# Kernel tuning notes

Measured on AMD Instinct MI355X. Metric: run time of the kernel, lower is better.

The kernel has to match this reference:

```python
import jax, jax.numpy as jnp
import numpy as np
import math

N_EDGES = 3
N_HEADS = 2
ITERS = 2
NEG = -1e9


def setup_inputs() -> dict:
    key = jax.random.key(0)
    ks = jax.random.split(key, 8)
    B, N, D = 4, 2048, 256
    E, H, I = N_EDGES, N_HEADS, ITERS
    s = 1.0 / math.sqrt(D)
    return {
        "nodes_embed": jax.random.normal(ks[0], (B, N, D), jnp.float32),
        "node_adj": jax.random.randint(ks[1], (B, N, N), 0, E + 1, jnp.int32),
        "Wq": jax.random.normal(ks[2], (E, D, D), jnp.float32) * s,
        "bq": jnp.zeros((E, D), jnp.float32),
        "Wk": jax.random.normal(ks[3], (E, D, D), jnp.float32) * s,
        "bk": jnp.zeros((E, D), jnp.float32),
        "gcn_W": jax.random.normal(ks[4], (I, D, D), jnp.float32) * s,
        "gcn_b": jnp.zeros((I, D), jnp.float32),
        "agg_W": jax.random.normal(ks[5], (H * D, D), jnp.float32) * (1.0 / math.sqrt(H * D)),
        "agg_b": jnp.zeros((D,), jnp.float32),
    }


def _forward(nodes_embed, node_adj, Wq, bq, Wk, bk, gcn_W, gcn_b, agg_W, agg_b):
    B, N, D = nodes_embed.shape
    H = N_HEADS
    dk = D // H
    adj = node_adj[:, None]  # [B,1,N,N] broadcast over heads

    # Per-edge-type masked attention accumulation (scores init at 0).
    scores = jnp.zeros((B, H, N, N), nodes_embed.dtype)
    for e in range(N_EDGES):  # small fixed edge-type loop
        q = (nodes_embed @ Wq[e] + bq[e]).reshape(B, N, H, dk).transpose(0, 2, 1, 3)
        k = (nodes_embed @ Wk[e] + bk[e]).reshape(B, N, H, dk).transpose(0, 2, 1, 3)
        raw = jnp.einsum('bhnd,bhmd->bhnm', q, k) / math.sqrt(dk)
        scores = jnp.where(adj == e + 1, scores + raw, scores)

    # Positions never touched (adj==0 or no matching type) stay exactly 0 -> masked.
    scores = jnp.where(scores == 0.0, NEG, scores)
    attn = jax.nn.softmax(scores, axis=-1)  # [B,H,N,N]

    # Per-head GCN stack (parameters shared across heads, as in the torch code).
    outs = []
    for head in range(H):
        a = attn[:, head]  # [B,N,N]
        degs = jnp.sum(a, axis=-1, keepdims=True)  # [B,N,1]
        x = nodes_embed
        for i in range(ITERS):
            h1 = jnp.einsum('bnd,df->bnf', x, gcn_W[i])
            sum_nei = jnp.einsum('bnm,bmf->bnf', a, h1)
            x = x + jax.nn.relu(sum_nei / degs + gcn_b[i])
        outs.append(x)

    out = jnp.concatenate(outs, axis=-1) @ agg_W + agg_b  # [B,N,D]
    graph_attention = jnp.transpose(attn, (1, 0, 2, 3))  # [H,B,N,N]
    return out, graph_attention


def reference(nodes_embed, node_adj, Wq, bq, Wk, bk, gcn_W, gcn_b, agg_W, agg_b):
    return _forward(nodes_embed, node_adj, Wq, bq, Wk, bk, gcn_W, gcn_b, agg_W, agg_b)
```

## Files before the change

kernel.cpp:

```cpp
#include <hip/hip_runtime.h>
#include <stdint.h>
#include <stddef.h>


typedef unsigned short bf16_t;
typedef __attribute__((ext_vector_type(4))) float floatx4;
typedef __attribute__((ext_vector_type(8))) __bf16 bf16x8;
typedef __attribute__((ext_vector_type(4))) unsigned short u16x4;

__device__ __forceinline__ bf16_t f2b(float f) {
  union { float f; uint32_t u; } v; v.f = f;
  uint32_t r = v.u + 0x7FFFu + ((v.u >> 16) & 1u);
  return (bf16_t)(r >> 16);
}
__device__ __forceinline__ float h2f(uint16_t u) {
  union { uint16_t u; _Float16 h; } v; v.u = u; return (float)v.h;
}
__device__ __forceinline__ uint16_t f2h(float f) {
  union { uint16_t u; _Float16 h; } v; v.h = (_Float16)f; return v.u;
}

typedef __attribute__((address_space(1))) void gvoid_t;
typedef __attribute__((address_space(3))) void svoid_t;
__device__ __forceinline__ void gll16(const void* g, void* l) {
  __builtin_amdgcn_global_load_lds((gvoid_t*)(g), (svoid_t*)(l), 16, 0, 0);
}


template <int NR>
__device__ __forceinline__ void stage128(const bf16_t* G, int ldg, bf16_t* L) {
  const int lane = threadIdx.x & 63, wave = threadIdx.x >> 6;
  const int li = lane >> 4, cp = lane & 15;
#pragma unroll
  for (int t = 0; t < NR / 16; ++t) {
    int base_r = wave * (NR / 4) + t * 4;
    int r = base_r + li;
    int cl = cp ^ (r & 15);
    gll16(G + (size_t)r * ldg + cl * 8, L + base_r * 128);
  }
}
template <int NR>
__device__ __forceinline__ void stage64(const bf16_t* G, int ldg, bf16_t* L) {
  const int lane = threadIdx.x & 63, wave = threadIdx.x >> 6;
  const int li = lane >> 3, cp = lane & 7;
#pragma unroll
  for (int t = 0; t < NR / 32; ++t) {
    int base_r = wave * (NR / 4) + t * 8;
    int r = base_r + li;
    int cl = cp ^ (r & 7);
    gll16(G + (size_t)r * ldg + cl * 8, L + base_r * 64);
  }
}
__device__ __forceinline__ bf16x8 frag128(const bf16_t* L, int row, int j, int quad) {
  int c = ((j << 2) + quad) ^ (row & 15);
  return *(const bf16x8*)(L + (row << 7) + (c << 3));
}
__device__ __forceinline__ bf16x8 frag64(const bf16_t* L, int row, int j, int quad) {
  int c = ((j << 2) + quad) ^ (row & 7);
  return *(const bf16x8*)(L + (row << 6) + (c << 3));
}

__device__ __forceinline__ bf16x8 lds_frag(const bf16_t* base, int row, int quad) {
  return *(const bf16x8*)(base + (row << 5) + (((quad + (row >> 1)) & 3) << 3));
}
__device__ __forceinline__ void gemm_core(
    const bf16_t* __restrict__ A, int lda, int rowA0,
    const bf16_t* __restrict__ Bt, int ldb, int rowB0,
    int K, bf16_t* lA, bf16_t* lB, floatx4 acc[4][4])
{
  const int lane = threadIdx.x & 63;
  const int wave = threadIdx.x >> 6;
  const int l16  = lane & 15;
  const int quad = lane >> 4;
  const int wm = (wave >> 1) << 6;
  const int wn = (wave & 1) << 6;
  const int srow = (wave << 5) + (lane >> 2);
  const int scol = (((lane & 3) - (srow >> 1)) & 3) << 3;
  const bf16_t* gA0 = A + (size_t)(rowA0 + srow) * lda + scol;
  const bf16_t* gA1 = gA0 + (size_t)16 * lda;
  const bf16_t* gB0 = Bt + (size_t)(rowB0 + srow) * ldb + scol;
  const bf16_t* gB1 = gB0 + (size_t)16 * ldb;
  bf16_t* lA0 = lA + (wave << 5) * 32;
  bf16_t* lA1 = lA0 + 16 * 32;
  bf16_t* lB0 = lB + (wave << 5) * 32;
  bf16_t* lB1 = lB0 + 16 * 32;

  for (int k0 = 0; k0 < K; k0 += 32) {
    __syncthreads();
    gll16(gA0 + k0, lA0);
    gll16(gA1 + k0, lA1);
    gll16(gB0 + k0, lB0);
    gll16(gB1 + k0, lB1);
    __syncthreads();
    bf16x8 af[4], bv[4];
#pragma unroll
    for (int mi = 0; mi < 4; ++mi) af[mi] = lds_frag(lA, wm + mi * 16 + l16, quad);
#pragma unroll
    for (int ni = 0; ni < 4; ++ni) bv[ni] = lds_frag(lB, wn + ni * 16 + l16, quad);
#pragma unroll
    for (int mi = 0; mi < 4; ++mi)
#pragma unroll
      for (int ni = 0; ni < 4; ++ni)
        acc[mi][ni] = __builtin_amdgcn_mfma_f32_16x16x32_bf16(af[mi], bv[ni], acc[mi][ni], 0, 0, 0);
  }
}

#define TILE_IDS \
  const int lane = threadIdx.x & 63; \
  const int wave = threadIdx.x >> 6; \
  const int l16  = lane & 15; \
  const int quad = lane >> 4; \
  const int wm = (wave >> 1) << 6; \
  const int wn = (wave & 1) << 6;

#define TILE_IDS64 \
  const int lane = threadIdx.x & 63; \
  const int wave = threadIdx.x >> 6; \
  const int l16  = lane & 15; \
  const int quad = lane >> 4; \
  const int wn = wave << 5;

#define ZERO44(acc) \
  { const floatx4 z4_ = {0.f, 0.f, 0.f, 0.f}; \
    for (int mi_ = 0; mi_ < 4; ++mi_) for (int ni_ = 0; ni_ < 4; ++ni_) acc[mi_][ni_] = z4_; }
#define ZERO42(acc) \
  { const floatx4 z4_ = {0.f, 0.f, 0.f, 0.f}; \
    for (int mi_ = 0; mi_ < 4; ++mi_) for (int ni_ = 0; ni_ < 2; ++ni_) acc[mi_][ni_] = z4_; }

__global__ __launch_bounds__(256) void k_cast_x(const float* __restrict__ x,
                                                bf16_t* __restrict__ xb) {
  int i = blockIdx.x * 256 + threadIdx.x;
  float4 a = ((const float4*)x)[i * 2];
  float4 b = ((const float4*)x)[i * 2 + 1];
  bf16_t o[8] = { f2b(a.x), f2b(a.y), f2b(a.z), f2b(a.w),
                  f2b(b.x), f2b(b.y), f2b(b.z), f2b(b.w) };
  ((uint4*)xb)[i] = *(uint4*)o;
}

__global__ __launch_bounds__(256) void k_cast_w(
    const float* __restrict__ Wq, const float* __restrict__ Wk,
    const float* __restrict__ gW, const float* __restrict__ aW,
    bf16_t* __restrict__ WqkT, bf16_t* __restrict__ gWT, bf16_t* __restrict__ aWT) {
  int idx = blockIdx.x * 256 + threadIdx.x;
  if (idx < 393216) {
    int zz = idx >> 16, r = idx & 65535;
    int n = r >> 8, k = r & 255;
    const float* src = (zz < 3) ? (Wq + (size_t)zz * 65536) : (Wk + (size_t)(zz - 3) * 65536);
    WqkT[idx] = f2b(src[k * 256 + n]);
  } else if (idx < 524288) {
    int t = idx - 393216;
    int i = t >> 16, r = t & 65535;
    int f = r >> 8, k = r & 255;
    gWT[t] = f2b(gW[(size_t)i * 65536 + k * 256 + f]);
  } else if (idx < 655360) {
    int t = idx - 524288;
    int f = t >> 9, k = t & 511;
    aWT[t] = f2b(aW[k * 256 + f]);
  }
}

__global__ __launch_bounds__(256) void k_gemm_proj(
    const bf16_t* __restrict__ xb, const bf16_t* __restrict__ WqkT,
    const float* __restrict__ bq, const float* __restrict__ bk,
    bf16_t* __restrict__ qcat, bf16_t* __restrict__ kcat) {
  __shared__ bf16_t lA[4096], lB[4096];
  int z = blockIdx.z;
  int e = (z < 3) ? z : z - 3;
  const bf16_t* Wz = WqkT + (size_t)z * 65536;
  const float* bias = ((z < 3) ? bq : bk) + e * 256;
  bf16_t* dst = (z < 3) ? qcat : kcat;
  int bm0 = blockIdx.y * 128, bn0 = blockIdx.x * 128;
  floatx4 acc[4][4];
  ZERO44(acc);
  gemm_core(xb, 256, bm0, Wz, 256, bn0, 256, lA, lB, acc);
  TILE_IDS;
#pragma unroll
  for (int mi = 0; mi < 4; ++mi)
#pragma unroll
    for (int ni = 0; ni < 4; ++ni)
#pragma unroll
      for (int r = 0; r < 4; ++r) {
        int row = bm0 + wm + mi * 16 + quad * 4 + r;
        int col = bn0 + wn + ni * 16 + l16;
        int b = row >> 11, n = row & 2047;
        int h = col >> 7, kk = col & 127;
        float v = acc[mi][ni][r] + bias[col];
        dst[((size_t)((b * 2 + h) * 2048 + n)) * 384 + e * 128 + kk] = f2b(v);
      }
}

__global__ __launch_bounds__(256) void k_scores(
    const bf16_t* __restrict__ qcat, const bf16_t* __restrict__ kcat,
    const int* __restrict__ adj, uint16_t* __restrict__ sc16) {
  __shared__ bf16_t lA[64 * 128];
  __shared__ bf16_t lB[128 * 128];
  int i = blockIdx.x;
  int z = i & 7, t = i >> 3;
  int y = t & 31, x = t >> 5;
  int h = z >> 2, b = z & 3;
  const bf16_t* A  = qcat + (size_t)(b * 2 + h) * 2048 * 384;
  const bf16_t* Bt = kcat + (size_t)(b * 2 + h) * 2048 * 384;
  const int* adjb = adj + (size_t)b * 2048 * 2048;
  int bm0 = y * 64, bn0 = x * 128;
  TILE_IDS64;

  uint32_t adjv[4][2];
#pragma unroll
  for (int mi = 0; mi < 4; ++mi)
#pragma unroll
    for (int ni = 0; ni < 2; ++ni) {
      int col = bn0 + wn + ni * 16 + l16;
      uint32_t v = 0;
#pragma unroll
      for (int r = 0; r < 4; ++r) {
        int row = bm0 + mi * 16 + quad * 4 + r;
        v |= ((uint32_t)adjb[(size_t)row * 2048 + col] & 3u) << (r * 8);
      }
      adjv[mi][ni] = v;
    }

  floatx4 sel[4][2];
  ZERO42(sel);
  for (int e = 0; e < 3; ++e) {
    __syncthreads();
    stage128<64>(A + (size_t)bm0 * 384 + e * 128, 384, lA);
    stage128<128>(Bt + (size_t)bn0 * 384 + e * 128, 384, lB);
    __syncthreads();
    floatx4 acc[4][2];
    ZERO42(acc);
#pragma unroll
    for (int j = 0; j < 4; ++j) {
      bf16x8 af[4], bv[2];
#pragma unroll
      for (int mi = 0; mi < 4; ++mi) af[mi] = frag128(lA, mi * 16 + l16, j, quad);
#pragma unroll
      for (int ni = 0; ni < 2; ++ni) bv[ni] = frag128(lB, wn + ni * 16 + l16, j, quad);
#pragma unroll
      for (int mi = 0; mi < 4; ++mi)
#pragma unroll
        for (int ni = 0; ni < 2; ++ni)
          acc[mi][ni] = __builtin_amdgcn_mfma_f32_16x16x32_bf16(af[mi], bv[ni], acc[mi][ni], 0, 0, 0);
    }
#pragma unroll
    for (int mi = 0; mi < 4; ++mi)
#pragma unroll
      for (int ni = 0; ni < 2; ++ni) {
        uint32_t av = adjv[mi][ni];
#pragma unroll
        for (int r = 0; r < 4; ++r) {
          bool m = (((av >> (r * 8)) & 255u) == (uint32_t)(e + 1));
          sel[mi][ni][r] = m ? acc[mi][ni][r] : sel[mi][ni][r];
        }
      }
  }
  const float scale = 0.08838834764831845f;
#pragma unroll
  for (int mi = 0; mi < 4; ++mi)
#pragma unroll
    for (int ni = 0; ni < 2; ++ni)
#pragma unroll
      for (int r = 0; r < 4; ++r) {
        int row = bm0 + mi * 16 + quad * 4 + r;
        int col = bn0 + wn + ni * 16 + l16;
        uint32_t a = (adjv[mi][ni] >> (r * 8)) & 255u;
        float v = (a == 0u) ? -60000.0f : sel[mi][ni][r] * scale;
        sc16[((size_t)z * 2048 + row) * 2048 + col] = f2h(v);
      }
}

__global__ __launch_bounds__(256) void k_softmax(uint16_t* sb, float* attn) {
  int row = blockIdx.x * 4 + (threadIdx.x >> 6);
  int lane = threadIdx.x & 63;
  uint16_t* p = sb + (size_t)row * 2048;
  float f[32];
  float mx = -3.4e38f;
#pragma unroll
  for (int j = 0; j < 4; ++j) {
    uint4 hv = ((const uint4*)p)[j * 64 + lane];
    const uint16_t* hu = (const uint16_t*)&hv;
#pragma unroll
    for (int q = 0; q < 8; ++q) {
      float v = h2f(hu[q]);
      f[j * 8 + q] = v;
      mx = fmaxf(mx, v);
    }
  }
#pragma unroll
  for (int off = 32; off; off >>= 1) mx = fmaxf(mx, __shfl_xor(mx, off));
  float s = 0.f;
#pragma unroll
  for (int k = 0; k < 32; ++k) { f[k] = __expf(f[k] - mx); s += f[k]; }
#pragma unroll
  for (int off = 32; off; off >>= 1) s += __shfl_xor(s, off);
  float inv = 1.0f / s;
  float* ar = attn + (size_t)row * 2048;
#pragma unroll
  for (int j = 0; j < 4; ++j) {
    float o[8];
#pragma unroll
    for (int q = 0; q < 8; ++q) o[q] = f[j * 8 + q] * inv;
    ((float4*)ar)[(j * 64 + lane) * 2 + 0] = *(float4*)&o[0];
    ((float4*)ar)[(j * 64 + lane) * 2 + 1] = *(float4*)&o[4];
    uint16_t ob[8];
#pragma unroll
    for (int q = 0; q < 8; ++q) ob[q] = f2b(o[q]);
    ((uint4*)p)[j * 64 + lane] = *(uint4*)ob;
  }
}

__global__ __launch_bounds__(256) void k_gemm_bf16T(
    const bf16_t* __restrict__ A, const bf16_t* __restrict__ Wt,
    bf16_t* __restrict__ CT) {
  __shared__ bf16_t lA[4096], lB[4096];
  int bm0 = blockIdx.y * 128, bn0 = blockIdx.x * 128;
  floatx4 acc[4][4];
  ZERO44(acc);
  gemm_core(A, 256, bm0, Wt, 256, bn0, 256, lA, lB, acc);
  TILE_IDS;
#pragma unroll
  for (int mi = 0; mi < 4; ++mi)
#pragma unroll
    for (int ni = 0; ni < 4; ++ni) {
      int row0 = bm0 + wm + mi * 16 + quad * 4;
      int col  = bn0 + wn + ni * 16 + l16;
      int s = row0 >> 11, n = row0 & 2047;
      u16x4 v = { f2b(acc[mi][ni][0]), f2b(acc[mi][ni][1]),
                  f2b(acc[mi][ni][2]), f2b(acc[mi][ni][3]) };
      *(u16x4*)&CT[(size_t)s * 524288 + (size_t)col * 2048 + n] = v;
    }
}

__global__ __launch_bounds__(256) void k_spmm(
    const bf16_t* __restrict__ abf, const bf16_t* __restrict__ h1T,
    long sBb, long sBh, const float* __restrict__ bias,
    const float* __restrict__ rin, long rib, long rih,
    float* __restrict__ rout,
    bf16_t* __restrict__ obf, long obb, long obh, int ldo) {
  __shared__ bf16_t lA[64 * 64];
  __shared__ bf16_t lB[128 * 64];
  int i = blockIdx.x;
  int z = i & 7, t = i >> 3;
  int x = t & 1, y = t >> 1;
  int h = z >> 2, b = z & 3;
  const bf16_t* A  = abf + (size_t)z * 2048 * 2048;
  const bf16_t* Bt = h1T + (size_t)b * sBb + (size_t)h * sBh;
  const float* rz  = rin + (size_t)b * rib + (size_t)h * rih;
  bf16_t* oz = obf + (size_t)b * obb + (size_t)h * obh;
  int bm0 = y * 64, bn0 = x * 128;
  TILE_IDS64;
  floatx4 acc[4][2];
  ZERO42(acc);
  for (int k0 = 0; k0 < 2048; k0 += 64) {
    __syncthreads();
    stage64<64>(A + (size_t)bm0 * 2048 + k0, 2048, lA);
    stage64<128>(Bt + (size_t)bn0 * 2048 + k0, 2048, lB);
    __syncthreads();
#pragma unroll
    for (int j = 0; j < 2; ++j) {
      bf16x8 af[4], bv[2];
#pragma unroll
      for (int mi = 0; mi < 4; ++mi) af[mi] = frag64(lA, mi * 16 + l16, j, quad);
#pragma unroll
      for (int ni = 0; ni < 2; ++ni) bv[ni] = frag64(lB, wn + ni * 16 + l16, j, quad);
#pragma unroll
      for (int mi = 0; mi < 4; ++mi)
#pragma unroll
        for (int ni = 0; ni < 2; ++ni)
          acc[mi][ni] = __builtin_amdgcn_mfma_f32_16x16x32_bf16(af[mi], bv[ni], acc[mi][ni], 0, 0, 0);
    }
  }
#pragma unroll
  for (int mi = 0; mi < 4; ++mi)
#pragma unroll
    for (int ni = 0; ni < 2; ++ni)
#pragma unroll
      for (int r = 0; r < 4; ++r) {
        int row = bm0 + mi * 16 + quad * 4 + r;
        int col = bn0 + wn + ni * 16 + l16;
        float s = acc[mi][ni][r] + bias[col];
        float xn = rz[(size_t)row * 256 + col] + fmaxf(s, 0.f);
        if (rout) rout[((size_t)z * 2048 + row) * 256 + col] = xn;
        oz[(size_t)row * ldo + col] = f2b(xn);
      }
}

__global__ __launch_bounds__(256) void k_final(
    const bf16_t* __restrict__ xcat, const bf16_t* __restrict__ aWT,
    const float* __restrict__ ab, float* __restrict__ out) {
  __shared__ bf16_t lA[4096], lB[4096];
  int bm0 = blockIdx.y * 128, bn0 = blockIdx.x * 128;
  floatx4 acc[4][4];
  ZERO44(acc);
  gemm_core(xcat, 512, bm0, aWT, 512, bn0, 512, lA, lB, acc);
  TILE_IDS;
#pragma unroll
  for (int mi = 0; mi < 4; ++mi)
#pragma unroll
    for (int ni = 0; ni < 4; ++ni)
#pragma unroll
      for (int r = 0; r < 4; ++r) {
        int row = bm0 + wm + mi * 16 + quad * 4 + r;
        int col = bn0 + wn + ni * 16 + l16;
        out[(size_t)row * 256 + col] = acc[mi][ni][r] + ab[col];
      }
}

extern "C" void kernel_launch(void* const* d_in, const int* in_sizes, int n_in,
                              void* d_out, int out_size, void* d_ws, size_t ws_size,
                              hipStream_t stream) {
  const float* x   = (const float*)d_in[0];
  const int*   adj = (const int*)d_in[1];
  const float* Wq  = (const float*)d_in[2];
  const float* bq  = (const float*)d_in[3];
  const float* Wk  = (const float*)d_in[4];
  const float* bk  = (const float*)d_in[5];
  const float* gW  = (const float*)d_in[6];
  const float* gb  = (const float*)d_in[7];
  const float* aW  = (const float*)d_in[8];
  const float* ab  = (const float*)d_in[9];
  float* out = (float*)d_out;
  float* sc  = out + 2097152;

  char* w = (char*)d_ws;
  bf16_t* xb   = (bf16_t*)w; w += 4194304;
  bf16_t* WqkT = (bf16_t*)w; w += 786432;
  bf16_t* gWT  = (bf16_t*)w; w += 262144;
  bf16_t* aWT  = (bf16_t*)w; w += 262144;
  bf16_t* qcat = (bf16_t*)w; w += 12582912;
  bf16_t* kcat = (bf16_t*)w; w += 12582912;
  bf16_t* abf  = (bf16_t*)w; w += 67108864;
  bf16_t* h1T  = (bf16_t*)w; w += 4194304;
  float*  x1   = (float*)w;  w += 16777216;
  bf16_t* x1b  = (bf16_t*)w; w += 8388608;
  bf16_t* h1T1 = qcat;
  bf16_t* xcat = kcat;

  k_cast_x<<<1024, 256, 0, stream>>>(x, xb);
  k_cast_w<<<2560, 256, 0, stream>>>(Wq, Wk, gW, aW, WqkT, gWT, aWT);
  k_gemm_proj<<<dim3(2, 64, 6), 256, 0, stream>>>(xb, WqkT, bq, bk, qcat, kcat);
  k_scores<<<4096, 256, 0, stream>>>(qcat, kcat, adj, (uint16_t*)abf);
  k_softmax<<<4096, 256, 0, stream>>>((uint16_t*)abf, sc);
  k_gemm_bf16T<<<dim3(2, 64, 1), 256, 0, stream>>>(xb, gWT, h1T);
  k_spmm<<<512, 256, 0, stream>>>(abf, h1T, 524288L, 0L, gb,
                                  x, 524288L, 0L, x1,
                                  x1b, 524288L, 2097152L, 256);
  k_gemm_bf16T<<<dim3(2, 128, 1), 256, 0, stream>>>(x1b, gWT + 65536, h1T1);
  k_spmm<<<512, 256, 0, stream>>>(abf, h1T1, 524288L, 2097152L, gb + 256,
                                  x1, 524288L, 2097152L, nullptr,
                                  xcat, 1048576L, 256L, 512);
  k_final<<<dim3(2, 64, 1), 256, 0, stream>>>(xcat, aWT, ab, out);
}
```

Measured before the change: 414.7 us.

## Double-buffer LDS staging in GEMM, scores and spmm kernels; nontemporal attn stores

Converts the shared GEMM core, the scores kernel and the spmm kernel to double-buffered LDS. The next k-tile is prefetched with global_load_lds while MFMAs run on the current buffer, which drops one barrier per iteration. The scores kernel now splits each 128-wide edge slice into two 64-wide stages so all six stages share one pipelined loop. The fp32 attention output stores become nontemporal. In exchange LDS use doubles, which may reduce occupancy, and the loop correctness depends on how async LDS loads and waitcnt interact with the single barrier.

New measurement: 453.8 us. +9.4%, slower.

```diff
diff --git a/kernel.cpp b/kernel.cpp
--- a/kernel.cpp
+++ b/kernel.cpp
@@ -27,18 +27,6 @@
 }
 
 
-template <int NR>
-__device__ __forceinline__ void stage128(const bf16_t* G, int ldg, bf16_t* L) {
-  const int lane = threadIdx.x & 63, wave = threadIdx.x >> 6;
-  const int li = lane >> 4, cp = lane & 15;
-#pragma unroll
-  for (int t = 0; t < NR / 16; ++t) {
-    int base_r = wave * (NR / 4) + t * 4;
-    int r = base_r + li;
-    int cl = cp ^ (r & 15);
-    gll16(G + (size_t)r * ldg + cl * 8, L + base_r * 128);
-  }
-}
 template <int NR>
 __device__ __forceinline__ void stage64(const bf16_t* G, int ldg, bf16_t* L) {
   const int lane = threadIdx.x & 63, wave = threadIdx.x >> 6;
@@ -50,10 +38,6 @@
     int cl = cp ^ (r & 7);
     gll16(G + (size_t)r * ldg + cl * 8, L + base_r * 64);
   }
-}
-__device__ __forceinline__ bf16x8 frag128(const bf16_t* L, int row, int j, int quad) {
-  int c = ((j << 2) + quad) ^ (row & 15);
-  return *(const bf16x8*)(L + (row << 7) + (c << 3));
 }
 __device__ __forceinline__ bf16x8 frag64(const bf16_t* L, int row, int j, int quad) {
   int c = ((j << 2) + quad) ^ (row & 7);
@@ -80,28 +64,40 @@
   const bf16_t* gA1 = gA0 + (size_t)16 * lda;
   const bf16_t* gB0 = Bt + (size_t)(rowB0 + srow) * ldb + scol;
   const bf16_t* gB1 = gB0 + (size_t)16 * ldb;
-  bf16_t* lA0 = lA + (wave << 5) * 32;
-  bf16_t* lA1 = lA0 + 16 * 32;
-  bf16_t* lB0 = lB + (wave << 5) * 32;
-  bf16_t* lB1 = lB0 + 16 * 32;
-
-  for (int k0 = 0; k0 < K; k0 += 32) {
-    __syncthreads();
-    gll16(gA0 + k0, lA0);
-    gll16(gA1 + k0, lA1);
-    gll16(gB0 + k0, lB0);
-    gll16(gB1 + k0, lB1);
-    __syncthreads();
+  const int soff = (wave << 5) * 32;
+
+  gll16(gA0, lA + soff);
+  gll16(gA1, lA + soff + 512);
+  gll16(gB0, lB + soff);
+  gll16(gB1, lB + soff + 512);
+  __syncthreads();
+
+  const int nk = K >> 5;
+  int cur = 0;
+  for (int t = 0; t < nk; ++t) {
+    if (t + 1 < nk) {
+      const int k1 = (t + 1) << 5;
+      bf16_t* nA = lA + ((cur ^ 1) << 12);
+      bf16_t* nB = lB + ((cur ^ 1) << 12);
+      gll16(gA0 + k1, nA + soff);
+      gll16(gA1 + k1, nA + soff + 512);
+      gll16(gB0 + k1, nB + soff);
+      gll16(gB1 + k1, nB + soff + 512);
+    }
+    const bf16_t* cA = lA + (cur << 12);
+    const bf16_t* cB = lB + (cur << 12);
     bf16x8 af[4], bv[4];
 #pragma unroll
-    for (int mi = 0; mi < 4; ++mi) af[mi] = lds_frag(lA, wm + mi * 16 + l16, quad);
-#pragma unroll
-    for (int ni = 0; ni < 4; ++ni) bv[ni] = lds_frag(lB, wn + ni * 16 + l16, quad);
+    for (int mi = 0; mi < 4; ++mi) af[mi] = lds_frag(cA, wm + mi * 16 + l16, quad);
+#pragma unroll
+    for (int ni = 0; ni < 4; ++ni) bv[ni] = lds_frag(cB, wn + ni * 16 + l16, quad);
 #pragma unroll
     for (int mi = 0; mi < 4; ++mi)
 #pragma unroll
       for (int ni = 0; ni < 4; ++ni)
         acc[mi][ni] = __builtin_amdgcn_mfma_f32_16x16x32_bf16(af[mi], bv[ni], acc[mi][ni], 0, 0, 0);
+    __syncthreads();
+    cur ^= 1;
   }
 }
 
@@ -163,7 +159,7 @@
     const bf16_t* __restrict__ xb, const bf16_t* __restrict__ WqkT,
     const float* __restrict__ bq, const float* __restrict__ bk,
     bf16_t* __restrict__ qcat, bf16_t* __restrict__ kcat) {
-  __shared__ bf16_t lA[4096], lB[4096];
+  __shared__ bf16_t lA[8192], lB[8192];
   int z = blockIdx.z;
   int e = (z < 3) ? z : z - 3;
   const bf16_t* Wz = WqkT + (size_t)z * 65536;
@@ -192,8 +188,8 @@
 __global__ __launch_bounds__(256) void k_scores(
     const bf16_t* __restrict__ qcat, const bf16_t* __restrict__ kcat,
     const int* __restrict__ adj, uint16_t* __restrict__ sc16) {
-  __shared__ bf16_t lA[64 * 128];
-  __shared__ bf16_t lB[128 * 128];
+  __shared__ bf16_t lA[2][64 * 64];
+  __shared__ bf16_t lB[2][128 * 64];
   int i = blockIdx.x;
   int z = i & 7, t = i >> 3;
   int y = t & 31, x = t >> 5;
@@ -219,39 +215,54 @@
       adjv[mi][ni] = v;
     }
 
+  const bf16_t* Ab = A + (size_t)bm0 * 384;
+  const bf16_t* Bb = Bt + (size_t)bn0 * 384;
+
+  stage64<64>(Ab, 384, lA[0]);
+  stage64<128>(Bb, 384, lB[0]);
+  __syncthreads();
+
   floatx4 sel[4][2];
+  floatx4 acc[4][2];
   ZERO42(sel);
-  for (int e = 0; e < 3; ++e) {
-    __syncthreads();
-    stage128<64>(A + (size_t)bm0 * 384 + e * 128, 384, lA);
-    stage128<128>(Bt + (size_t)bn0 * 384 + e * 128, 384, lB);
-    __syncthreads();
-    floatx4 acc[4][2];
-    ZERO42(acc);
-#pragma unroll
-    for (int j = 0; j < 4; ++j) {
+  ZERO42(acc);
+  int cur = 0;
+  for (int s = 0; s < 6; ++s) {
+    if (s + 1 < 6) {
+      int off = (s + 1) << 6;
+      stage64<64>(Ab + off, 384, lA[cur ^ 1]);
+      stage64<128>(Bb + off, 384, lB[cur ^ 1]);
+    }
+#pragma unroll
+    for (int j = 0; j < 2; ++j) {
       bf16x8 af[4], bv[2];
 #pragma unroll
-      for (int mi = 0; mi < 4; ++mi) af[mi] = frag128(lA, mi * 16 + l16, j, quad);
-#pragma unroll
-      for (int ni = 0; ni < 2; ++ni) bv[ni] = frag128(lB, wn + ni * 16 + l16, j, quad);
+      for (int mi = 0; mi < 4; ++mi) af[mi] = frag64(lA[cur], mi * 16 + l16, j, quad);
+#pragma unroll
+      for (int ni = 0; ni < 2; ++ni) bv[ni] = frag64(lB[cur], wn + ni * 16 + l16, j, quad);
 #pragma unroll
       for (int mi = 0; mi < 4; ++mi)
 #pragma unroll
         for (int ni = 0; ni < 2; ++ni)
           acc[mi][ni] = __builtin_amdgcn_mfma_f32_16x16x32_bf16(af[mi], bv[ni], acc[mi][ni], 0, 0, 0);
     }
-#pragma unroll
-    for (int mi = 0; mi < 4; ++mi)
-#pragma unroll
-      for (int ni = 0; ni < 2; ++ni) {
-        uint32_t av = adjv[mi][ni];
-#pragma unroll
-        for (int r = 0; r < 4; ++r) {
-          bool m = (((av >> (r * 8)) & 255u) == (uint32_t)(e + 1));
-          sel[mi][ni][r] = m ? acc[mi][ni][r] : sel[mi][ni][r];
+    if (s & 1) {
+      int e = s >> 1;
+#pragma unroll
+      for (int mi = 0; mi < 4; ++mi)
+#pragma unroll
+        for (int ni = 0; ni < 2; ++ni) {
+          uint32_t av = adjv[mi][ni];
+#pragma unroll
+          for (int r = 0; r < 4; ++r) {
+            bool m = (((av >> (r * 8)) & 255u) == (uint32_t)(e + 1));
+            sel[mi][ni][r] = m ? acc[mi][ni][r] : sel[mi][ni][r];
+          }
         }
-      }
+      ZERO42(acc);
+    }
+    __syncthreads();
+    cur ^= 1;
   }
   const float scale = 0.08838834764831845f;
 #pragma unroll
@@ -293,14 +304,14 @@
 #pragma unroll
   for (int off = 32; off; off >>= 1) s += __shfl_xor(s, off);
   float inv = 1.0f / s;
-  float* ar = attn + (size_t)row * 2048;
+  floatx4* ar = (floatx4*)(attn + (size_t)row * 2048);
 #pragma unroll
   for (int j = 0; j < 4; ++j) {
     float o[8];
 #pragma unroll
     for (int q = 0; q < 8; ++q) o[q] = f[j * 8 + q] * inv;
-    ((float4*)ar)[(j * 64 + lane) * 2 + 0] = *(float4*)&o[0];
-    ((float4*)ar)[(j * 64 + lane) * 2 + 1] = *(float4*)&o[4];
+    __builtin_nontemporal_store(*(floatx4*)&o[0], ar + (j * 64 + lane) * 2 + 0);
+    __builtin_nontemporal_store(*(floatx4*)&o[4], ar + (j * 64 + lane) * 2 + 1);
     uint16_t ob[8];
 #pragma unroll
     for (int q = 0; q < 8; ++q) ob[q] = f2b(o[q]);
@@ -311,7 +322,7 @@
 __global__ __launch_bounds__(256) void k_gemm_bf16T(
     const bf16_t* __restrict__ A, const bf16_t* __restrict__ Wt,
     bf16_t* __restrict__ CT) {
-  __shared__ bf16_t lA[4096], lB[4096];
+  __shared__ bf16_t lA[8192], lB[8192];
   int bm0 = blockIdx.y * 128, bn0 = blockIdx.x * 128;
   floatx4 acc[4][4];
   ZERO44(acc);
@@ -336,8 +347,8 @@
     const float* __restrict__ rin, long rib, long rih,
     float* __restrict__ rout,
     bf16_t* __restrict__ obf, long obb, long obh, int ldo) {
-  __shared__ bf16_t lA[64 * 64];
-  __shared__ bf16_t lB[128 * 64];
+  __shared__ bf16_t lA[2][64 * 64];
+  __shared__ bf16_t lB[2][128 * 64];
   int i = blockIdx.x;
   int z = i & 7, t = i >> 3;
   int x = t & 1, y = t >> 1;
@@ -348,26 +359,37 @@
   bf16_t* oz = obf + (size_t)b * obb + (size_t)h * obh;
   int bm0 = y * 64, bn0 = x * 128;
   TILE_IDS64;
+  const bf16_t* Ab = A + (size_t)bm0 * 2048;
+  const bf16_t* Bb = Bt + (size_t)bn0 * 2048;
+
+  stage64<64>(Ab, 2048, lA[0]);
+  stage64<128>(Bb, 2048, lB[0]);
+  __syncthreads();
+
   floatx4 acc[4][2];
   ZERO42(acc);
-  for (int k0 = 0; k0 < 2048; k0 += 64) {
-    __syncthreads();
-    stage64<64>(A + (size_t)bm0 * 2048 + k0, 2048, lA);
-    stage64<128>(Bt + (size_t)bn0 * 2048 + k0, 2048, lB);
-    __syncthreads();
+  int cur = 0;
+  for (int kt = 0; kt < 32; ++kt) {
+    if (kt + 1 < 32) {
+      int k1 = (kt + 1) << 6;
+      stage64<64>(Ab + k1, 2048, lA[cur ^ 1]);
+      stage64<128>(Bb + k1, 2048, lB[cur ^ 1]);
+    }
 #pragma unroll
     for (int j = 0; j < 2; ++j) {
       bf16x8 af[4], bv[2];
 #pragma unroll
-      for (int mi = 0; mi < 4; ++mi) af[mi] = frag64(lA, mi * 16 + l16, j, quad);
-#pragma unroll
-      for (int ni = 0; ni < 2; ++ni) bv[ni] = frag64(lB, wn + ni * 16 + l16, j, quad);
+      for (int mi = 0; mi < 4; ++mi) af[mi] = frag64(lA[cur], mi * 16 + l16, j, quad);
+#pragma unroll
+      for (int ni = 0; ni < 2; ++ni) bv[ni] = frag64(lB[cur], wn + ni * 16 + l16, j, quad);
 #pragma unroll
       for (int mi = 0; mi < 4; ++mi)
 #pragma unroll
         for (int ni = 0; ni < 2; ++ni)
           acc[mi][ni] = __builtin_amdgcn_mfma_f32_16x16x32_bf16(af[mi], bv[ni], acc[mi][ni], 0, 0, 0);
     }
+    __syncthreads();
+    cur ^= 1;
   }
 #pragma unroll
   for (int mi = 0; mi < 4; ++mi)
@@ -387,7 +409,7 @@
 __global__ __launch_bounds__(256) void k_final(
     const bf16_t* __restrict__ xcat, const bf16_t* __restrict__ aWT,
     const float* __restrict__ ab, float* __restrict__ out) {
-  __shared__ bf16_t lA[4096], lB[4096];
+  __shared__ bf16_t lA[8192], lB[8192];
   int bm0 = blockIdx.y * 128, bn0 = blockIdx.x * 128;
   floatx4 acc[4][4];
   ZERO44(acc);
```

## Merge cast kernels, fold first GCN GEMM into projection, share adj across heads

Applied to the files above, without the earlier changes.

Merges the input and weight cast kernels into one launch and folds the first-iteration GCN projection (x @ gcn_W[0]) into the Q/K projection kernel as an extra z-slice, removing two launches. The scores kernel now handles both heads per block, so each adjacency tile is loaded once and reused for both heads instead of read twice. In exchange, the scores grid is halved, so each block does twice the work with less parallelism, and the projection epilogue gains a branch.

Result: no change. 420.9 us (+1.5%).

```diff
diff --git a/kernel.cpp b/kernel.cpp
--- a/kernel.cpp
+++ b/kernel.cpp
@@ -127,33 +127,35 @@
   { const floatx4 z4_ = {0.f, 0.f, 0.f, 0.f}; \
     for (int mi_ = 0; mi_ < 4; ++mi_) for (int ni_ = 0; ni_ < 2; ++ni_) acc[mi_][ni_] = z4_; }
 
-__global__ __launch_bounds__(256) void k_cast_x(const float* __restrict__ x,
-                                                bf16_t* __restrict__ xb) {
-  int i = blockIdx.x * 256 + threadIdx.x;
-  float4 a = ((const float4*)x)[i * 2];
-  float4 b = ((const float4*)x)[i * 2 + 1];
-  bf16_t o[8] = { f2b(a.x), f2b(a.y), f2b(a.z), f2b(a.w),
-                  f2b(b.x), f2b(b.y), f2b(b.z), f2b(b.w) };
-  ((uint4*)xb)[i] = *(uint4*)o;
-}
-
-__global__ __launch_bounds__(256) void k_cast_w(
+__global__ __launch_bounds__(256) void k_cast(
+    const float* __restrict__ x,
     const float* __restrict__ Wq, const float* __restrict__ Wk,
     const float* __restrict__ gW, const float* __restrict__ aW,
+    bf16_t* __restrict__ xb,
     bf16_t* __restrict__ WqkT, bf16_t* __restrict__ gWT, bf16_t* __restrict__ aWT) {
   int idx = blockIdx.x * 256 + threadIdx.x;
-  if (idx < 393216) {
-    int zz = idx >> 16, r = idx & 65535;
+  if (idx < 262144) {
+    int i = idx;
+    float4 a = ((const float4*)x)[i * 2];
+    float4 b = ((const float4*)x)[i * 2 + 1];
+    bf16_t o[8] = { f2b(a.x), f2b(a.y), f2b(a.z), f2b(a.w),
+                    f2b(b.x), f2b(b.y), f2b(b.z), f2b(b.w) };
+    ((uint4*)xb)[i] = *(uint4*)o;
+    return;
+  }
+  int t0 = idx - 262144;
+  if (t0 < 393216) {
+    int zz = t0 >> 16, r = t0 & 65535;
     int n = r >> 8, k = r & 255;
     const float* src = (zz < 3) ? (Wq + (size_t)zz * 65536) : (Wk + (size_t)(zz - 3) * 65536);
-    WqkT[idx] = f2b(src[k * 256 + n]);
-  } else if (idx < 524288) {
-    int t = idx - 393216;
+    WqkT[t0] = f2b(src[k * 256 + n]);
+  } else if (t0 < 524288) {
+    int t = t0 - 393216;
     int i = t >> 16, r = t & 65535;
     int f = r >> 8, k = r & 255;
     gWT[t] = f2b(gW[(size_t)i * 65536 + k * 256 + f]);
-  } else if (idx < 655360) {
-    int t = idx - 524288;
+  } else if (t0 < 655360) {
+    int t = t0 - 524288;
     int f = t >> 9, k = t & 511;
     aWT[t] = f2b(aW[k * 256 + f]);
   }
@@ -161,32 +163,48 @@
 
 __global__ __launch_bounds__(256) void k_gemm_proj(
     const bf16_t* __restrict__ xb, const bf16_t* __restrict__ WqkT,
+    const bf16_t* __restrict__ gWT,
     const float* __restrict__ bq, const float* __restrict__ bk,
-    bf16_t* __restrict__ qcat, bf16_t* __restrict__ kcat) {
+    bf16_t* __restrict__ qcat, bf16_t* __restrict__ kcat,
+    bf16_t* __restrict__ h1T) {
   __shared__ bf16_t lA[4096], lB[4096];
   int z = blockIdx.z;
-  int e = (z < 3) ? z : z - 3;
-  const bf16_t* Wz = WqkT + (size_t)z * 65536;
-  const float* bias = ((z < 3) ? bq : bk) + e * 256;
-  bf16_t* dst = (z < 3) ? qcat : kcat;
+  const bf16_t* Wz = (z < 6) ? (WqkT + (size_t)z * 65536) : gWT;
   int bm0 = blockIdx.y * 128, bn0 = blockIdx.x * 128;
   floatx4 acc[4][4];
   ZERO44(acc);
   gemm_core(xb, 256, bm0, Wz, 256, bn0, 256, lA, lB, acc);
   TILE_IDS;
-#pragma unroll
-  for (int mi = 0; mi < 4; ++mi)
-#pragma unroll
-    for (int ni = 0; ni < 4; ++ni)
-#pragma unroll
-      for (int r = 0; r < 4; ++r) {
-        int row = bm0 + wm + mi * 16 + quad * 4 + r;
-        int col = bn0 + wn + ni * 16 + l16;
-        int b = row >> 11, n = row & 2047;
-        int h = col >> 7, kk = col & 127;
-        float v = acc[mi][ni][r] + bias[col];
-        dst[((size_t)((b * 2 + h) * 2048 + n)) * 384 + e * 128 + kk] = f2b(v);
+  if (z < 6) {
+    int e = (z < 3) ? z : z - 3;
+    const float* bias = ((z < 3) ? bq : bk) + e * 256;
+    bf16_t* dst = (z < 3) ? qcat : kcat;
+#pragma unroll
+    for (int mi = 0; mi < 4; ++mi)
+#pragma unroll
+      for (int ni = 0; ni < 4; ++ni)
+#pragma unroll
+        for (int r = 0; r < 4; ++r) {
+          int row = bm0 + wm + mi * 16 + quad * 4 + r;
+          int col = bn0 + wn + ni * 16 + l16;
+          int b = row >> 11, n = row & 2047;
+          int h = col >> 7, kk = col & 127;
+          float v = acc[mi][ni][r] + bias[col];
+          dst[((size_t)((b * 2 + h) * 2048 + n)) * 384 + e * 128 + kk] = f2b(v);
+        }
+  } else {
+#pragma unroll
+    for (int mi = 0; mi < 4; ++mi)
+#pragma unroll
+      for (int ni = 0; ni < 4; ++ni) {
+        int row0 = bm0 + wm + mi * 16 + quad * 4;
+        int col  = bn0 + wn + ni * 16 + l16;
+        int s = row0 >> 11, n = row0 & 2047;
+        u16x4 v = { f2b(acc[mi][ni][0]), f2b(acc[mi][ni][1]),
+                    f2b(acc[mi][ni][2]), f2b(acc[mi][ni][3]) };
+        *(u16x4*)&h1T[(size_t)s * 524288 + (size_t)col * 2048 + n] = v;
       }
+  }
 }
 
 __global__ __launch_bounds__(256) void k_scores(
@@ -195,11 +213,8 @@
   __shared__ bf16_t lA[64 * 128];
   __shared__ bf16_t lB[128 * 128];
   int i = blockIdx.x;
-  int z = i & 7, t = i >> 3;
+  int b = i & 3, t = i >> 2;
   int y = t & 31, x = t >> 5;
-  int h = z >> 2, b = z & 3;
-  const bf16_t* A  = qcat + (size_t)(b * 2 + h) * 2048 * 384;
-  const bf16_t* Bt = kcat + (size_t)(b * 2 + h) * 2048 * 384;
   const int* adjb = adj + (size_t)b * 2048 * 2048;
   int bm0 = y * 64, bn0 = x * 128;
   TILE_IDS64;
@@ -219,53 +234,58 @@
       adjv[mi][ni] = v;
     }
 
-  floatx4 sel[4][2];
-  ZERO42(sel);
-  for (int e = 0; e < 3; ++e) {
-    __syncthreads();
-    stage128<64>(A + (size_t)bm0 * 384 + e * 128, 384, lA);
-    stage128<128>(Bt + (size_t)bn0 * 384 + e * 128, 384, lB);
-    __syncthreads();
-    floatx4 acc[4][2];
-    ZERO42(acc);
-#pragma unroll
-    for (int j = 0; j < 4; ++j) {
-      bf16x8 af[4], bv[2];
-#pragma unroll
-      for (int mi = 0; mi < 4; ++mi) af[mi] = frag128(lA, mi * 16 + l16, j, quad);
-#pragma unroll
-      for (int ni = 0; ni < 2; ++ni) bv[ni] = frag128(lB, wn + ni * 16 + l16, j, quad);
+  const float scale = 0.08838834764831845f;
+  for (int h = 0; h < 2; ++h) {
+    const bf16_t* A  = qcat + (size_t)(b * 2 + h) * 2048 * 384;
+    const bf16_t* Bt = kcat + (size_t)(b * 2 + h) * 2048 * 384;
+    floatx4 sel[4][2];
+    ZERO42(sel);
+    for (int e = 0; e < 3; ++e) {
+      __syncthreads();
+      stage128<64>(A + (size_t)bm0 * 384 + e * 128, 384, lA);
+      stage128<128>(Bt + (size_t)bn0 * 384 + e * 128, 384, lB);
+      __syncthreads();
+      floatx4 acc[4][2];
+      ZERO42(acc);
+#pragma unroll
+      for (int j = 0; j < 4; ++j) {
+        bf16x8 af[4], bv[2];
+#pragma unroll
+        for (int mi = 0; mi < 4; ++mi) af[mi] = frag128(lA, mi * 16 + l16, j, quad);
+#pragma unroll
+        for (int ni = 0; ni < 2; ++ni) bv[ni] = frag128(lB, wn + ni * 16 + l16, j, quad);
+#pragma unroll
+        for (int mi = 0; mi < 4; ++mi)
+#pragma unroll
+          for (int ni = 0; ni < 2; ++ni)
+            acc[mi][ni] = __builtin_amdgcn_mfma_f32_16x16x32_bf16(af[mi], bv[ni], acc[mi][ni], 0, 0, 0);
+      }
 #pragma unroll
       for (int mi = 0; mi < 4; ++mi)
 #pragma unroll
-        for (int ni = 0; ni < 2; ++ni)
-          acc[mi][ni] = __builtin_amdgcn_mfma_f32_16x16x32_bf16(af[mi], bv[ni], acc[mi][ni], 0, 0, 0);
+        for (int ni = 0; ni < 2; ++ni) {
+          uint32_t av = adjv[mi][ni];
+#pragma unroll
+          for (int r = 0; r < 4; ++r) {
+            bool m = (((av >> (r * 8)) & 255u) == (uint32_t)(e + 1));
+            sel[mi][ni][r] = m ? acc[mi][ni][r] : sel[mi][ni][r];
+          }
+        }
     }
+    size_t zslice = (size_t)(h * 4 + b) * 2048;
 #pragma unroll
     for (int mi = 0; mi < 4; ++mi)
 #pragma unroll
-      for (int ni = 0; ni < 2; ++ni) {
-        uint32_t av = adjv[mi][ni];
+      for (int ni = 0; ni < 2; ++ni)
 #pragma unroll
         for (int r = 0; r < 4; ++r) {
-          bool m = (((av >> (r * 8)) & 255u) == (uint32_t)(e + 1));
-          sel[mi][ni][r] = m ? acc[mi][ni][r] : sel[mi][ni][r];
+          int row = bm0 + mi * 16 + quad * 4 + r;
+          int col = bn0 + wn + ni * 16 + l16;
+          uint32_t a = (adjv[mi][ni] >> (r * 8)) & 255u;
+          float v = (a == 0u) ? -60000.0f : sel[mi][ni][r] * scale;
+          sc16[(zslice + row) * 2048 + col] = f2h(v);
         }
-      }
-  }
-  const float scale = 0.08838834764831845f;
-#pragma unroll
-  for (int mi = 0; mi < 4; ++mi)
-#pragma unroll
-    for (int ni = 0; ni < 2; ++ni)
-#pragma unroll
-      for (int r = 0; r < 4; ++r) {
-        int row = bm0 + mi * 16 + quad * 4 + r;
-        int col = bn0 + wn + ni * 16 + l16;
-        uint32_t a = (adjv[mi][ni] >> (r * 8)) & 255u;
-        float v = (a == 0u) ? -60000.0f : sel[mi][ni][r] * scale;
-        sc16[((size_t)z * 2048 + row) * 2048 + col] = f2h(v);
-      }
+  }
 }
 
 __global__ __launch_bounds__(256) void k_softmax(uint16_t* sb, float* attn) {
@@ -435,12 +455,11 @@
   bf16_t* h1T1 = qcat;
   bf16_t* xcat = kcat;
 
-  k_cast_x<<<1024, 256, 0, stream>>>(x, xb);
-  k_cast_w<<<2560, 256, 0, stream>>>(Wq, Wk, gW, aW, WqkT, gWT, aWT);
-  k_gemm_proj<<<dim3(2, 64, 6), 256, 0, stream>>>(xb, WqkT, bq, bk, qcat, kcat);
-  k_scores<<<4096, 256, 0, stream>>>(qcat, kcat, adj, (uint16_t*)abf);
+  k_cast<<<3584, 256, 0, stream>>>(x, Wq, Wk, gW, aW, xb, WqkT, gWT, aWT);
+  k_gemm_proj<<<dim3(2, 64, 7), 256, 0, stream>>>(xb, WqkT, gWT, bq, bk,
+                                                  qcat, kcat, h1T);
+  k_scores<<<2048, 256, 0, stream>>>(qcat, kcat, adj, (uint16_t*)abf);
   k_softmax<<<4096, 256, 0, stream>>>((uint16_t*)abf, sc);
-  k_gemm_bf16T<<<dim3(2, 64, 1), 256, 0, stream>>>(xb, gWT, h1T);
   k_spmm<<<512, 256, 0, stream>>>(abf, h1T, 524288L, 0L, gb,
                                   x, 524288L, 0L, x1,
                                   x1b, 524288L, 2097152L, 256);
```
